# Optimization experiments

Hardware: AMD Instinct MI355X
Metric: run time of the kernel (lower is better)

The kernel has to match this reference:

```python
import jax, jax.numpy as jnp
import numpy as np
import math

B, L, NV, PRED = 8, 512, 32, 96
D, PL, STRIDE = 128, 16, 8
E, TOPN, H = 8, 2, 512
P = (L - PL) // STRIDE + 2  # 64 patches (includes replication pad of STRIDE)
BAL_COEF, Z_COEF = 0.01, 0.001


def sinusoid_pe(n, d):
    pos = np.arange(n, dtype=np.float32)[:, None]
    div = np.exp(np.arange(0, d, 2, dtype=np.float32) * -(math.log(10000.0) / d))
    pe = np.zeros((n, d), dtype=np.float32)
    pe[:, 0::2] = np.sin(pos * div)
    pe[:, 1::2] = np.cos(pos * div)
    return jnp.asarray(pe)


def setup_inputs() -> dict:
    key = jax.random.key(0)
    ks = jax.random.split(key, 10)
    return {
        "x_enc": jax.random.normal(ks[0], (B, L, NV), jnp.float32),
        "x_mark_enc": jax.random.normal(ks[1], (B, L, 4), jnp.float32),
        "x_dec": jnp.zeros((B, 144, NV), jnp.float32),
        "x_mark_dec": jnp.zeros((B, 144, 4), jnp.float32),
        "W_patch": jax.random.normal(ks[2], (PL, D), jnp.float32) * 0.05,
        "Wg": jax.random.normal(ks[3], (D, E), jnp.float32) * 0.05,
        "W1": jax.random.normal(ks[4], (E, D, H), jnp.float32) * 0.05,
        "b1": jnp.zeros((E, H), jnp.float32),
        "W2": jax.random.normal(ks[5], (E, H, D), jnp.float32) * 0.05,
        "b2": jnp.zeros((E, D), jnp.float32),
        "W_head": jax.random.normal(ks[6], (D * P, PRED), jnp.float32) * 0.02,
        "b_head": jnp.zeros((PRED,), jnp.float32),
    }


def _forward(x_enc, W_patch, Wg, W1, b1, W2, b2, W_head, b_head):
    # instance norm over time (detached stats, like the torch code)
    means = jax.lax.stop_gradient(jnp.mean(x_enc, axis=1, keepdims=True))
    xc = x_enc - means
    stdev = jax.lax.stop_gradient(
        jnp.sqrt(jnp.mean((x_enc - means) ** 2, axis=1, keepdims=True) + 1e-5))
    xc = xc / stdev
    # [B, NV, L] -> replication pad right by STRIDE -> unfold into patches
    x = jnp.transpose(xc, (0, 2, 1))
    xp = jnp.pad(x, ((0, 0), (0, 0), (0, STRIDE)), mode="edge")
    idx = jnp.arange(P)[:, None] * STRIDE + jnp.arange(PL)[None, :]  # [P, PL]
    patches = xp[:, :, idx]  # [B, NV, P, PL]
    tok = patches.reshape(B * NV, P, PL)
    h = jnp.einsum("tpl,ld->tpd", tok, W_patch) + sinusoid_pe(P, D)[None]
    # ---- MoE over flattened tokens ----
    N = B * NV * P
    xf = h.reshape(N, D)
    logits = xf @ Wg                              # [N, E]
    probs = jax.nn.softmax(logits, axis=-1)
    gates, tops = jax.lax.top_k(probs, TOPN)      # [N, TOPN]
    # dense per-expert FFN (exact GELU, as nn.GELU default)
    eh = jax.nn.gelu(jnp.einsum("nd,edh->neh", xf, W1) + b1, approximate=False)
    eo = jnp.einsum("neh,ehd->ned", eh, W2) + b2  # [N, E, D]
    onehot = jax.nn.one_hot(tops, E, dtype=xf.dtype)          # [N, TOPN, E]
    cw = jnp.einsum("nk,nke->ne", gates, onehot)              # combine weights
    y = jnp.einsum("ne,ned->nd", cw, eo)
    # aux losses: load-balance + router z-loss
    mask = onehot.sum(axis=1)                                  # [N, E]
    balance = E * jnp.sum(jnp.mean(probs, axis=0) * jnp.mean(mask, axis=0)) / TOPN
    zloss = jnp.mean(jax.nn.logsumexp(logits, axis=-1) ** 2)
    aux = BAL_COEF * balance + Z_COEF * zloss
    # ---- head ----
    enc = y.reshape(B, NV, P, D).transpose(0, 1, 3, 2)         # [B, NV, D, P]
    flat = enc.reshape(B, NV, D * P)
    dec = flat @ W_head + b_head                               # [B, NV, PRED]
    dec = jnp.transpose(dec, (0, 2, 1))                        # [B, PRED, NV]
    dec = dec * stdev[:, 0, :][:, None, :] + means[:, 0, :][:, None, :]
    return dec, aux


def reference(x_enc, x_mark_enc, x_dec, x_mark_dec, W_patch, Wg, W1, b1, W2, b2,
              W_head, b_head):
    return _forward(x_enc, W_patch, Wg, W1, b1, W2, b2, W_head, b_head)
```

## Files before the change

### kernel.cpp

```cpp
#include <hip/hip_runtime.h>
#include <math.h>


typedef __attribute__((ext_vector_type(8))) short bf16x8;
typedef __attribute__((ext_vector_type(4))) float f32x4;

__device__ __forceinline__ float bf2f(unsigned short u){
  unsigned x = ((unsigned)u) << 16; float f; __builtin_memcpy(&f, &x, 4); return f;
}
__device__ __forceinline__ unsigned short f2bf(float f){
  unsigned x; __builtin_memcpy(&x, &f, 4);
  return (unsigned short)((x + 0x7FFFu + ((x >> 16) & 1u)) >> 16);
}
__device__ __forceinline__ float ldin(const void* p, int i, int f32){
  return f32 ? ((const float*)p)[i] : bf2f(((const unsigned short*)p)[i]);
}
__device__ __forceinline__ void stout(void* p, int i, float v, int f32){
  if (f32) ((float*)p)[i] = v; else ((unsigned short*)p)[i] = f2bf(v);
}
__device__ __forceinline__ f32x4 mfma16(bf16x8 a, bf16x8 b, f32x4 c){
  return __builtin_amdgcn_mfma_f32_16x16x32_bf16(a, b, c, 0, 0, 0);
}
#define BAR_RAW() asm volatile("s_waitcnt lgkmcnt(0)\n\ts_barrier" ::: "memory")
__device__ __forceinline__ float gelu_fast(float v){
  float u = v*v;
  float inner = v * fmaf(0.044715f, u, 1.0f);
  float e = __expf(-1.5957691216f * inner);
  return v / (1.0f + e);
}

#define OFF_CNT    0
#define OFF_SUMS   64
#define OFF_MEANS  256
#define OFF_STDS   1280
#define OFF_ECNT   2304
#define OFF_PE     3328
#define OFF_W1T    134400
#define OFF_W2T    1182976
#define OFF_WHT    2231552
#define OFF_CW     3804416
#define OFF_XFBF   4328704
#define OFF_FLATB  8523008
#define OFF_EO     12717312
#define OFF_TOKSLOT 79826176
#define OFF_DECP   79957248

__global__ __launch_bounds__(256) void k_detect(const unsigned short* __restrict__ xe,
                                                int* cnt){
  __shared__ int sc;
  int t = threadIdx.x;
  if (t == 0) sc = 0;
  __syncthreads();
  int c = 0;
  int base = blockIdx.x * 2048;
  for (int k = 0; k < 8; ++k){
    unsigned short u = xe[base + k*256 + t];
    int ex = (u >> 7) & 0xFF;
    if (ex == 0xFF || (ex == 0 && (u & 0x7F))) c++;
  }
  atomicAdd(&sc, c);
  __syncthreads();
  if (t == 0 && sc) atomicAdd(cnt, sc);
}

__global__ __launch_bounds__(256) void k_prep_tr(const void* __restrict__ W1,
                                                 const void* __restrict__ W2,
                                                 const void* __restrict__ Wh,
                                                 const int* cnt, float* pe,
                                                 unsigned short* W1T, unsigned short* W2T,
                                                 unsigned short* WhT){
  int t = threadIdx.x;
  if (blockIdx.x == 0){
    for (int i = t; i < 8192; i += 256){
      int p = i >> 7, d = i & 127;
      float freq = __expf(-(float)(d & ~1) * 0.07195578415606394f);
      float ang = (float)p * freq;
      pe[i] = (d & 1) ? __cosf(ang) : __sinf(ang);
    }
    return;
  }
  int f32 = (cnt[0] >= 4);
  __shared__ float tile[32*33];
  int tb = blockIdx.x - 1;
  int r = t >> 3, cg = (t & 7) * 4;
  const void* src; unsigned short* dst;
  int in0, instride, out0, outstride;
  if (tb < 512){
    int e = tb >> 6, ti = tb & 63, d0 = (ti & 3) * 32, h0 = (ti >> 2) * 32;
    src = W1; dst = W1T;
    in0 = e*65536 + d0*512 + h0; instride = 512;
    out0 = e*65536 + h0*128 + d0; outstride = 128;
  } else if (tb < 1024){
    int tc = tb - 512;
    int e = tc >> 6, ti = tc & 63, d0 = (ti & 3) * 32, h0 = (ti >> 2) * 32;
    src = W2; dst = W2T;
    in0 = e*65536 + h0*128 + d0; instride = 128;
    out0 = e*65536 + d0*512 + h0; outstride = 512;
  } else {
    int tc = tb - 1024;
    int kt = tc / 3, nt = tc - kt*3;
    int k0 = kt*32, n0 = nt*32;
    src = Wh; dst = WhT;
    in0 = k0*96 + n0; instride = 96;
    out0 = n0*8192 + k0; outstride = 8192;
  }
  #pragma unroll
  for (int j = 0; j < 4; ++j)
    tile[r*33 + cg + j] = ldin(src, in0 + r*instride + cg + j, f32);
  __syncthreads();
  ushort4 o;
  o.x = f2bf(tile[(cg+0)*33 + r]);
  o.y = f2bf(tile[(cg+1)*33 + r]);
  o.z = f2bf(tile[(cg+2)*33 + r]);
  o.w = f2bf(tile[(cg+3)*33 + r]);
  *(ushort4*)(dst + out0 + r*outstride + cg) = o;
}

__global__ __launch_bounds__(256) void k_embed(const void* __restrict__ xe,
                                               const void* __restrict__ Wp,
                                               const void* __restrict__ Wg,
                                               const int* cnt,
                                               const float* __restrict__ peg,
                                               float* means, float* stds,
                                               unsigned short* xfbf, float* cwg,
                                               float* sums,
                                               int* ecnt, int* elist, int* tokslot){
  __shared__ float xn[512];
  __shared__ float WpL[2048];
  __shared__ float WgL[1024];
  __shared__ float Xf[8192];
  __shared__ float lp[1024];
  __shared__ float taux[576];
  __shared__ float reds[256], redss[256];
  __shared__ float msh[2];
  __shared__ int lcnt[8], lbase[8];

  int bv = blockIdx.x;
  int b = bv >> 5, v = bv & 31;
  int t = threadIdx.x;
  int f32 = (cnt[0] >= 4);

  if (t < 8) lcnt[t] = 0;

  float x0 = ldin(xe, (b*512 + t)*32 + v, f32);
  float x1 = ldin(xe, (b*512 + t + 256)*32 + v, f32);
  xn[t] = x0; xn[t+256] = x1;
  reds[t] = x0 + x1; redss[t] = x0*x0 + x1*x1;
  #pragma unroll
  for (int it = 0; it < 8; ++it)
    WpL[it*256 + t] = ldin(Wp, it*256 + t, f32);
  #pragma unroll
  for (int j = 0; j < 4; ++j)
    WgL[j*256 + t] = ldin(Wg, j*256 + t, f32);
  __syncthreads();
  for (int s = 128; s > 0; s >>= 1){
    if (t < s){ reds[t] += reds[t+s]; redss[t] += redss[t+s]; }
    __syncthreads();
  }
  if (t == 0){
    float m = reds[0] / 512.f;
    float sd = sqrtf(redss[0] / 512.f - m*m + 1e-5f);
    msh[0] = m; msh[1] = 1.f / sd;
    means[bv] = m; stds[bv] = sd;
  }
  __syncthreads();
  float mean = msh[0], rstd = msh[1];
  xn[t] = (xn[t] - mean) * rstd;
  xn[t+256] = (xn[t+256] - mean) * rstd;
  __syncthreads();
  {
    int p = t >> 2, q = t & 3;
    float tv[16];
    #pragma unroll
    for (int l = 0; l < 16; ++l){
      int xi = p*8 + l; if (xi > 511) xi = 511;
      tv[l] = xn[xi];
    }
    for (int dd = 0; dd < 32; ++dd){
      int d = q*32 + dd;
      float acc = peg[p*128 + d];
      #pragma unroll
      for (int l = 0; l < 16; ++l) acc += tv[l] * WpL[l*128 + d];
      Xf[p*128 + d] = acc;
    }
  }
  __syncthreads();
  if (t < 128){
    int p = t >> 1, half = t & 1;
    float s[8] = {0,0,0,0,0,0,0,0};
    for (int d = half*64; d < half*64 + 64; ++d){
      float xv = Xf[p*128 + d];
      #pragma unroll
      for (int e = 0; e < 8; ++e) s[e] += xv * WgL[d*8 + e];
    }
    #pragma unroll
    for (int e = 0; e < 8; ++e) lp[(p*2 + half)*8 + e] = s[e];
  }
  __syncthreads();
  int bi = 0, si = 0, lo0 = 0, lo1 = 0;
  if (t < 64){
    int p = t;
    float lg[8];
    #pragma unroll
    for (int e = 0; e < 8; ++e) lg[e] = lp[(p*2)*8 + e] + lp[(p*2+1)*8 + e];
    float m = lg[0];
    #pragma unroll
    for (int e = 1; e < 8; ++e) m = fmaxf(m, lg[e]);
    float pr[8]; float se = 0.f;
    #pragma unroll
    for (int e = 0; e < 8; ++e){ pr[e] = __expf(lg[e] - m); se += pr[e]; }
    float inv = 1.f / se;
    float lse = m + logf(se);
    #pragma unroll
    for (int e = 0; e < 8; ++e) pr[e] *= inv;
    float best = -1.f;
    #pragma unroll
    for (int e = 0; e < 8; ++e) if (pr[e] > best){ best = pr[e]; bi = e; }
    float sec = -1.f;
    #pragma unroll
    for (int e = 0; e < 8; ++e) if (e != bi && pr[e] > sec){ sec = pr[e]; si = e; }
    #pragma unroll
    for (int e = 0; e < 8; ++e){
      float w = (e == bi) ? best : ((e == si) ? sec : 0.f);
      cwg[(bv*64 + p)*8 + e] = w;
      taux[p*9 + e] = pr[e];
    }
    taux[p*9 + 8] = lse * lse;
    lp[p] = (float)bi; lp[64 + p] = (float)si;
    lo0 = atomicAdd(&lcnt[bi], 1);
    lo1 = atomicAdd(&lcnt[si], 1);
  }
  __syncthreads();
  if (t < 8) lbase[t] = atomicAdd(ecnt + t*32, lcnt[t]);
  __syncthreads();
  if (t < 64){
    int n = bv*64 + t;
    int p0 = lbase[bi] + lo0, p1 = lbase[si] + lo1;
    elist[bi*16384 + p0] = n;
    elist[si*16384 + p1] = n;
    tokslot[n*2]     = (bi << 14) + p0;
    tokslot[n*2 + 1] = (si << 14) + p1;
  }
  if (t < 17){
    float s = 0.f;
    if (t < 8){ for (int p = 0; p < 64; ++p) s += taux[p*9 + t]; }
    else if (t < 16){
      int e = t - 8;
      for (int p = 0; p < 64; ++p)
        s += ((int)lp[p] == e || (int)lp[64+p] == e) ? 1.f : 0.f;
    }
    else { for (int p = 0; p < 64; ++p) s += taux[p*9 + 8]; }
    atomicAdd(sums + t, s);
  }
  #pragma unroll
  for (int pass = 0; pass < 4; ++pass){
    int idx = pass*256 + t;
    int base = idx*8;
    bf16x8 o;
    #pragma unroll
    for (int j = 0; j < 8; ++j) o[j] = (short)f2bf(Xf[base + j]);
    *(bf16x8*)(xfbf + bv*8192 + base) = o;
  }
}

__global__ __launch_bounds__(256, 3) void k_moe(const unsigned short* __restrict__ xfbf,
                                                const unsigned short* __restrict__ W1T,
                                                const unsigned short* __restrict__ W2T,
                                                const void* __restrict__ b1g,
                                                const int* cnt,
                                                const float* __restrict__ cwg,
                                                const int* __restrict__ ecnt,
                                                const int* __restrict__ elist,
                                                float* __restrict__ Eo){
  __shared__ __align__(16) char lds[49664];
  short* Xs  = (short*)(lds);
  short* Bu1 = (short*)(lds + 8704);
  short* Bu2 = (short*)(lds + 26112);
  short* Ag  = (short*)(lds + 44544);
  float* cws = (float*)(lds + 49152);
  int*   lsn = (int*)(lds + 49280);

  int t = threadIdx.x;
  int e = 8, ti = 0;
  {
    int acc = 0, bk = blockIdx.x;
    #pragma unroll
    for (int ee = 0; ee < 8; ++ee){
      int tl = (ecnt[ee*32] + 31) >> 5;
      if (e == 8 && bk < acc + tl){ e = ee; ti = bk - acc; }
      acc += tl;
    }
  }
  if (e == 8) return;
  int cntE = ecnt[e*32];
  int tbase = ti*32;

  int f32 = (cnt[0] >= 4);
  int wave = t >> 6, lane = t & 63;
  int quad = lane >> 4, li = lane & 15;
  int c1 = wave * 16;
  int c2 = wave * 32;

  const unsigned short* W1e = W1T + e*65536;
  const unsigned short* W2e = W2T + e*65536;

  bf16x8 pf1[4], pf2[4];
  #pragma unroll
  for (int pass = 0; pass < 4; ++pass){
    int idx = pass*64 + lane;
    int row = idx >> 4, kg = idx & 15;
    pf1[pass] = *(const bf16x8*)(W1e + (c1 + row)*128 + kg*8);
  }
  #pragma unroll
  for (int pass = 0; pass < 4; ++pass){
    int idx = pass*64 + lane;
    int row = idx >> 3, kg = idx & 7;
    pf2[pass] = *(const bf16x8*)(W2e + (c2 + row)*512 + kg*8);
  }

  if (t < 32){
    int ok = (tbase + t) < cntE;
    int n = ok ? elist[e*16384 + tbase + t] : 0;
    lsn[t] = n;
    cws[t] = ok ? cwg[n*8 + e] : 0.f;
  }
  __syncthreads();
  #pragma unroll
  for (int pass = 0; pass < 2; ++pass){
    int idx = pass*256 + t;
    int row = idx >> 4, kg = idx & 15;
    int n = lsn[row];
    *(bf16x8*)(Xs + row*136 + kg*8) =
      *(const bf16x8*)(xfbf + n*128 + kg*8);
  }
  float cwv[2][4];
  #pragma unroll
  for (int rt = 0; rt < 2; ++rt)
    #pragma unroll
    for (int r = 0; r < 4; ++r)
      cwv[rt][r] = cws[rt*16 + quad*4 + r];
  __syncthreads();

  f32x4 Yacc[2][2];
  #pragma unroll
  for (int a = 0; a < 2; ++a)
    #pragma unroll
    for (int bb = 0; bb < 2; ++bb){ f32x4 z = {0.f,0.f,0.f,0.f}; Yacc[a][bb] = z; }

  for (int hc = 0; hc < 8; ++hc){
    #pragma unroll
    for (int pass = 0; pass < 4; ++pass){
      int idx = pass*64 + lane;
      int row = idx >> 4, kg = idx & 15;
      *(bf16x8*)(Bu1 + (c1 + row)*136 + kg*8) = pf1[pass];
    }
    #pragma unroll
    for (int pass = 0; pass < 4; ++pass){
      int idx = pass*64 + lane;
      int row = idx >> 3, kg = idx & 7;
      *(bf16x8*)(Bu2 + (c2 + row)*72 + kg*8) = pf2[pass];
    }
    float bias = ldin(b1g, e*512 + hc*64 + c1 + li, f32);
    if (hc < 7){
      #pragma unroll
      for (int pass = 0; pass < 4; ++pass){
        int idx = pass*64 + lane;
        int row = idx >> 4, kg = idx & 15;
        pf1[pass] = *(const bf16x8*)(W1e + ((hc+1)*64 + c1 + row)*128 + kg*8);
      }
      #pragma unroll
      for (int pass = 0; pass < 4; ++pass){
        int idx = pass*64 + lane;
        int row = idx >> 3, kg = idx & 7;
        pf2[pass] = *(const bf16x8*)(W2e + (c2 + row)*512 + (hc+1)*64 + kg*8);
      }
    }
    f32x4 acc1[2];
    { f32x4 z = {0.f,0.f,0.f,0.f}; acc1[0] = z; acc1[1] = z; }
    #pragma unroll
    for (int ks = 0; ks < 4; ++ks){
      int kk = ks*32 + quad*8;
      bf16x8 a0 = *(const bf16x8*)(Xs + li*136 + kk);
      bf16x8 a1 = *(const bf16x8*)(Xs + (16 + li)*136 + kk);
      bf16x8 b0 = *(const bf16x8*)(Bu1 + (c1 + li)*136 + kk);
      acc1[0] = mfma16(a0, b0, acc1[0]);
      acc1[1] = mfma16(a1, b0, acc1[1]);
    }
    BAR_RAW();
    #pragma unroll
    for (int rt = 0; rt < 2; ++rt){
      #pragma unroll
      for (int r = 0; r < 4; ++r){
        int row = rt*16 + quad*4 + r;
        float g = gelu_fast(acc1[rt][r] + bias);
        Ag[row*72 + c1 + li] = (short)f2bf(g * cwv[rt][r]);
      }
    }
    BAR_RAW();
    #pragma unroll
    for (int ks = 0; ks < 2; ++ks){
      int kk = ks*32 + quad*8;
      bf16x8 a0 = *(const bf16x8*)(Ag + li*72 + kk);
      bf16x8 a1 = *(const bf16x8*)(Ag + (16 + li)*72 + kk);
      #pragma unroll
      for (int ct = 0; ct < 2; ++ct){
        bf16x8 bb = *(const bf16x8*)(Bu2 + (c2 + ct*16 + li)*72 + kk);
        Yacc[0][ct] = mfma16(a0, bb, Yacc[0][ct]);
        Yacc[1][ct] = mfma16(a1, bb, Yacc[1][ct]);
      }
    }
  }
  #pragma unroll
  for (int ct = 0; ct < 2; ++ct){
    int col = c2 + ct*16 + li;
    #pragma unroll
    for (int rt = 0; rt < 2; ++rt)
      #pragma unroll
      for (int r = 0; r < 4; ++r){
        int row = rt*16 + quad*4 + r;
        if (tbase + row < cntE)
          Eo[(size_t)((e << 14) + tbase + row)*128 + col] = Yacc[rt][ct][r];
      }
  }
}

__global__ __launch_bounds__(256) void k_flat(const float* __restrict__ Eo,
                                              const int* __restrict__ tokslot,
                                              const float* __restrict__ cwg,
                                              const void* __restrict__ b2g,
                                              const int* cnt,
                                              unsigned short* __restrict__ flatb){
  __shared__ float Yl[64*130];
  __shared__ float b2f[1024];
  __shared__ float cwl[512];
  __shared__ int tsl[128];
  int bv = blockIdx.x;
  int t = threadIdx.x;
  int f32 = (cnt[0] >= 4);
  if (t < 64){
    int2 v = *(const int2*)(tokslot + (bv*64 + t)*2);
    tsl[t*2] = v.x; tsl[t*2+1] = v.y;
  }
  #pragma unroll
  for (int j = 0; j < 4; ++j) b2f[j*256 + t] = ldin(b2g, j*256 + t, f32);
  #pragma unroll
  for (int j = 0; j < 2; ++j) cwl[j*256 + t] = cwg[bv*512 + j*256 + t];
  __syncthreads();
  #pragma unroll
  for (int pass = 0; pass < 32; ++pass){
    int idx = pass*256 + t;
    int row = idx >> 7, col = idx & 127;
    Yl[row*130 + col] = Eo[(size_t)tsl[row*2]*128 + col]
                      + Eo[(size_t)tsl[row*2+1]*128 + col];
  }
  __syncthreads();
  int d = t >> 1, ph = (t & 1) * 32;
  float b2c[8];
  #pragma unroll
  for (int e = 0; e < 8; ++e) b2c[e] = b2f[e*128 + d];
  unsigned short ob[32];
  for (int j = 0; j < 32; ++j){
    int p = ph + j;
    float add = 0.f;
    #pragma unroll
    for (int e = 0; e < 8; ++e) add += cwl[p*8 + e] * b2c[e];
    ob[j] = f2bf(Yl[p*130 + d] + add);
  }
  #pragma unroll
  for (int m = 0; m < 4; ++m)
    *(bf16x8*)(flatb + bv*8192 + d*64 + ph + m*8) = *(bf16x8*)(ob + m*8);
}

__global__ __launch_bounds__(256) void k_head(const unsigned short* __restrict__ flatb,
                                              const unsigned short* __restrict__ WhT,
                                              float* __restrict__ dec_part){
  int t = threadIdx.x;
  int mt = blockIdx.x & 15, kc = blockIdx.x >> 4;
  int wave = t >> 6, lane = t & 63, quad = lane >> 4, li = lane & 15;
  int kbase = kc*512 + wave*128;
  f32x4 acc[6];
  #pragma unroll
  for (int nt = 0; nt < 6; ++nt){ f32x4 z = {0.f,0.f,0.f,0.f}; acc[nt] = z; }
  #pragma unroll
  for (int ks = 0; ks < 4; ++ks){
    int k = kbase + ks*32 + quad*8;
    bf16x8 a = *(const bf16x8*)(flatb + (mt*16 + li)*8192 + k);
    #pragma unroll
    for (int nt = 0; nt < 6; ++nt){
      bf16x8 b = *(const bf16x8*)(WhT + (nt*16 + li)*8192 + k);
      acc[nt] = mfma16(a, b, acc[nt]);
    }
  }
  __shared__ float redsh[4][16][96];
  #pragma unroll
  for (int nt = 0; nt < 6; ++nt)
    #pragma unroll
    for (int r = 0; r < 4; ++r)
      redsh[wave][quad*4 + r][nt*16 + li] = acc[nt][r];
  __syncthreads();
  #pragma unroll
  for (int u = 0; u < 6; ++u){
    int o = t*6 + u;
    int row = o / 96, col = o % 96;
    float s = redsh[0][row][col] + redsh[1][row][col] + redsh[2][row][col] + redsh[3][row][col];
    dec_part[kc*24576 + (mt*16 + row)*96 + col] = s;
  }
}

__global__ __launch_bounds__(256) void k_final(const float* __restrict__ dec_part,
                                               const void* __restrict__ bh,
                                               const int* cnt,
                                               const float* __restrict__ means,
                                               const float* __restrict__ stds,
                                               const float* __restrict__ sums,
                                               void* out){
  int o = blockIdx.x*256 + threadIdx.x;
  int f32 = (cnt[0] >= 4);
  int b = o / 3072, rem = o % 3072, j = rem >> 5, v = rem & 31;
  int bv = b*32 + v;
  int idx = bv*96 + j;
  float s = 0.f;
  #pragma unroll
  for (int kc = 0; kc < 16; ++kc) s += dec_part[kc*24576 + idx];
  float val = (s + ldin(bh, j, f32)) * stds[bv] + means[bv];
  stout(out, o, val, f32);
  if (o == 0){
    float bal = 0.f;
    for (int e = 0; e < 8; ++e) bal += (sums[e] / 16384.f) * (sums[8+e] / 16384.f);
    bal = 8.f * bal / 2.f;
    float aux = 0.01f * bal + 0.001f * (sums[16] / 16384.f);
    stout(out, 24576, aux, f32);
  }
}

extern "C" void kernel_launch(void* const* d_in, const int* in_sizes, int n_in,
                              void* d_out, int out_size, void* d_ws, size_t ws_size,
                              hipStream_t stream){
  const void* xe = d_in[0];
  const void* Wp = d_in[4];
  const void* Wg = d_in[5];
  const void* W1 = d_in[6];
  const void* b1 = d_in[7];
  const void* W2 = d_in[8];
  const void* b2 = d_in[9];
  const void* Wh = d_in[10];
  const void* bh = d_in[11];

  char* ws = (char*)d_ws;
  int*   cnt   = (int*)(ws + OFF_CNT);
  float* sums  = (float*)(ws + OFF_SUMS);
  float* means = (float*)(ws + OFF_MEANS);
  float* stds  = (float*)(ws + OFF_STDS);
  int*   ecnt  = (int*)(ws + OFF_ECNT);
  float* pe    = (float*)(ws + OFF_PE);
  unsigned short* W1T   = (unsigned short*)(ws + OFF_W1T);
  unsigned short* W2T   = (unsigned short*)(ws + OFF_W2T);
  unsigned short* WhT   = (unsigned short*)(ws + OFF_WHT);
  float* cw    = (float*)(ws + OFF_CW);
  unsigned short* xfbf  = (unsigned short*)(ws + OFF_XFBF);
  unsigned short* flatb = (unsigned short*)(ws + OFF_FLATB);
  int*   elist = (int*)(ws + OFF_FLATB);
  float* Eo    = (float*)(ws + OFF_EO);
  int*   tokslot = (int*)(ws + OFF_TOKSLOT);
  float* dec_part = (float*)(ws + OFF_DECP);

  hipMemsetAsync(ws, 0, 3328, stream);
  k_detect<<<64, 256, 0, stream>>>((const unsigned short*)xe, cnt);
  k_prep_tr<<<1793, 256, 0, stream>>>(W1, W2, Wh, cnt, pe, W1T, W2T, WhT);
  k_embed<<<256, 256, 0, stream>>>(xe, Wp, Wg, cnt, pe, means, stds,
                                   xfbf, cw, sums, ecnt, elist, tokslot);
  k_moe<<<1032, 256, 0, stream>>>(xfbf, W1T, W2T, b1, cnt, cw, ecnt, elist, Eo);
  k_flat<<<256, 256, 0, stream>>>(Eo, tokslot, cw, b2, cnt, flatb);
  k_head<<<256, 256, 0, stream>>>(flatb, WhT, dec_part);
  k_final<<<96, 256, 0, stream>>>(dec_part, bh, cnt, means, stds, sums, d_out);
}
```

Before: 159.0 us.

## Drop dtype-detect kernel and load MoE weights directly into registers

Removes the k_detect launch and instead picks the fp32/bf16 input path on the host from the input byte size. It also restructures k_moe so W1/W2 fragments and token rows are read straight from global memory into MFMA operand registers, with W1 double-buffered across h-chunks. This drops the LDS staging buffers and one barrier, shrinking shared memory from about 49KB to about 5KB and allowing higher occupancy. In exchange, each wave issues more scattered global loads, and the dtype choice now relies on the input size convention.

Measured after the change: 163.9 us. 1.03x slower.

```diff
diff --git a/kernel.cpp b/kernel.cpp
--- a/kernel.cpp
+++ b/kernel.cpp
@@ -29,7 +29,6 @@
   return v / (1.0f + e);
 }
 
-#define OFF_CNT    0
 #define OFF_SUMS   64
 #define OFF_MEANS  256
 #define OFF_STDS   1280
@@ -45,28 +44,10 @@
 #define OFF_TOKSLOT 79826176
 #define OFF_DECP   79957248
 
-__global__ __launch_bounds__(256) void k_detect(const unsigned short* __restrict__ xe,
-                                                int* cnt){
-  __shared__ int sc;
-  int t = threadIdx.x;
-  if (t == 0) sc = 0;
-  __syncthreads();
-  int c = 0;
-  int base = blockIdx.x * 2048;
-  for (int k = 0; k < 8; ++k){
-    unsigned short u = xe[base + k*256 + t];
-    int ex = (u >> 7) & 0xFF;
-    if (ex == 0xFF || (ex == 0 && (u & 0x7F))) c++;
-  }
-  atomicAdd(&sc, c);
-  __syncthreads();
-  if (t == 0 && sc) atomicAdd(cnt, sc);
-}
-
 __global__ __launch_bounds__(256) void k_prep_tr(const void* __restrict__ W1,
                                                  const void* __restrict__ W2,
                                                  const void* __restrict__ Wh,
-                                                 const int* cnt, float* pe,
+                                                 int f32, float* pe,
                                                  unsigned short* W1T, unsigned short* W2T,
                                                  unsigned short* WhT){
   int t = threadIdx.x;
@@ -79,7 +60,6 @@
     }
     return;
   }
-  int f32 = (cnt[0] >= 4);
   __shared__ float tile[32*33];
   int tb = blockIdx.x - 1;
   int r = t >> 3, cg = (t & 7) * 4;
@@ -119,7 +99,7 @@
 __global__ __launch_bounds__(256) void k_embed(const void* __restrict__ xe,
                                                const void* __restrict__ Wp,
                                                const void* __restrict__ Wg,
-                                               const int* cnt,
+                                               int f32,
                                                const float* __restrict__ peg,
                                                float* means, float* stds,
                                                unsigned short* xfbf, float* cwg,
@@ -138,7 +118,6 @@
   int bv = blockIdx.x;
   int b = bv >> 5, v = bv & 31;
   int t = threadIdx.x;
-  int f32 = (cnt[0] >= 4);
 
   if (t < 8) lcnt[t] = 0;
 
@@ -267,18 +246,14 @@
                                                 const unsigned short* __restrict__ W1T,
                                                 const unsigned short* __restrict__ W2T,
                                                 const void* __restrict__ b1g,
-                                                const int* cnt,
+                                                int f32,
                                                 const float* __restrict__ cwg,
                                                 const int* __restrict__ ecnt,
                                                 const int* __restrict__ elist,
                                                 float* __restrict__ Eo){
-  __shared__ __align__(16) char lds[49664];
-  short* Xs  = (short*)(lds);
-  short* Bu1 = (short*)(lds + 8704);
-  short* Bu2 = (short*)(lds + 26112);
-  short* Ag  = (short*)(lds + 44544);
-  float* cws = (float*)(lds + 49152);
-  int*   lsn = (int*)(lds + 49280);
+  __shared__ __align__(16) short Ag[32*72];
+  __shared__ float cws[32];
+  __shared__ int   lsn[32];
 
   int t = threadIdx.x;
   int e = 8, ti = 0;
@@ -295,7 +270,6 @@
   int cntE = ecnt[e*32];
   int tbase = ti*32;
 
-  int f32 = (cnt[0] >= 4);
   int wave = t >> 6, lane = t & 63;
   int quad = lane >> 4, li = lane & 15;
   int c1 = wave * 16;
@@ -304,19 +278,12 @@
   const unsigned short* W1e = W1T + e*65536;
   const unsigned short* W2e = W2T + e*65536;
 
-  bf16x8 pf1[4], pf2[4];
-  #pragma unroll
-  for (int pass = 0; pass < 4; ++pass){
-    int idx = pass*64 + lane;
-    int row = idx >> 4, kg = idx & 15;
-    pf1[pass] = *(const bf16x8*)(W1e + (c1 + row)*128 + kg*8);
-  }
-  #pragma unroll
-  for (int pass = 0; pass < 4; ++pass){
-    int idx = pass*64 + lane;
-    int row = idx >> 3, kg = idx & 7;
-    pf2[pass] = *(const bf16x8*)(W2e + (c2 + row)*512 + kg*8);
-  }
+  bf16x8 w1f[2][4];
+  float biasv[2];
+  #pragma unroll
+  for (int ks = 0; ks < 4; ++ks)
+    w1f[0][ks] = *(const bf16x8*)(W1e + (c1 + li)*128 + ks*32 + quad*8);
+  biasv[0] = ldin(b1g, e*512 + c1 + li, f32);
 
   if (t < 32){
     int ok = (tbase + t) < cntE;
@@ -324,14 +291,15 @@
     lsn[t] = n;
     cws[t] = ok ? cwg[n*8 + e] : 0.f;
   }
-  __syncthreads();
-  #pragma unroll
-  for (int pass = 0; pass < 2; ++pass){
-    int idx = pass*256 + t;
-    int row = idx >> 4, kg = idx & 15;
-    int n = lsn[row];
-    *(bf16x8*)(Xs + row*136 + kg*8) =
-      *(const bf16x8*)(xfbf + n*128 + kg*8);
+  BAR_RAW();
+
+  int n0 = lsn[li], n1 = lsn[16 + li];
+  bf16x8 a0[4], a1[4];
+  #pragma unroll
+  for (int ks = 0; ks < 4; ++ks){
+    int kk = ks*32 + quad*8;
+    a0[ks] = *(const bf16x8*)(xfbf + n0*128 + kk);
+    a1[ks] = *(const bf16x8*)(xfbf + n1*128 + kk);
   }
   float cwv[2][4];
   #pragma unroll
@@ -339,7 +307,6 @@
     #pragma unroll
     for (int r = 0; r < 4; ++r)
       cwv[rt][r] = cws[rt*16 + quad*4 + r];
-  __syncthreads();
 
   f32x4 Yacc[2][2];
   #pragma unroll
@@ -347,67 +314,48 @@
     #pragma unroll
     for (int bb = 0; bb < 2; ++bb){ f32x4 z = {0.f,0.f,0.f,0.f}; Yacc[a][bb] = z; }
 
+  #pragma unroll
   for (int hc = 0; hc < 8; ++hc){
-    #pragma unroll
-    for (int pass = 0; pass < 4; ++pass){
-      int idx = pass*64 + lane;
-      int row = idx >> 4, kg = idx & 15;
-      *(bf16x8*)(Bu1 + (c1 + row)*136 + kg*8) = pf1[pass];
-    }
-    #pragma unroll
-    for (int pass = 0; pass < 4; ++pass){
-      int idx = pass*64 + lane;
-      int row = idx >> 3, kg = idx & 7;
-      *(bf16x8*)(Bu2 + (c2 + row)*72 + kg*8) = pf2[pass];
-    }
-    float bias = ldin(b1g, e*512 + hc*64 + c1 + li, f32);
+    const int cur = hc & 1, nxt = cur ^ 1;
+    bf16x8 w2f[2][2];
+    #pragma unroll
+    for (int ks = 0; ks < 2; ++ks)
+      #pragma unroll
+      for (int ct = 0; ct < 2; ++ct)
+        w2f[ks][ct] = *(const bf16x8*)(W2e + (c2 + ct*16 + li)*512 + hc*64 + ks*32 + quad*8);
     if (hc < 7){
       #pragma unroll
-      for (int pass = 0; pass < 4; ++pass){
-        int idx = pass*64 + lane;
-        int row = idx >> 4, kg = idx & 15;
-        pf1[pass] = *(const bf16x8*)(W1e + ((hc+1)*64 + c1 + row)*128 + kg*8);
-      }
-      #pragma unroll
-      for (int pass = 0; pass < 4; ++pass){
-        int idx = pass*64 + lane;
-        int row = idx >> 3, kg = idx & 7;
-        pf2[pass] = *(const bf16x8*)(W2e + (c2 + row)*512 + (hc+1)*64 + kg*8);
-      }
-    }
-    f32x4 acc1[2];
-    { f32x4 z = {0.f,0.f,0.f,0.f}; acc1[0] = z; acc1[1] = z; }
+      for (int ks = 0; ks < 4; ++ks)
+        w1f[nxt][ks] = *(const bf16x8*)(W1e + ((hc+1)*64 + c1 + li)*128 + ks*32 + quad*8);
+      biasv[nxt] = ldin(b1g, e*512 + (hc+1)*64 + c1 + li, f32);
+    }
+    f32x4 acc1a = {0.f,0.f,0.f,0.f}, acc1b = {0.f,0.f,0.f,0.f};
     #pragma unroll
     for (int ks = 0; ks < 4; ++ks){
-      int kk = ks*32 + quad*8;
-      bf16x8 a0 = *(const bf16x8*)(Xs + li*136 + kk);
-      bf16x8 a1 = *(const bf16x8*)(Xs + (16 + li)*136 + kk);
-      bf16x8 b0 = *(const bf16x8*)(Bu1 + (c1 + li)*136 + kk);
-      acc1[0] = mfma16(a0, b0, acc1[0]);
-      acc1[1] = mfma16(a1, b0, acc1[1]);
+      acc1a = mfma16(a0[ks], w1f[cur][ks], acc1a);
+      acc1b = mfma16(a1[ks], w1f[cur][ks], acc1b);
     }
     BAR_RAW();
-    #pragma unroll
-    for (int rt = 0; rt < 2; ++rt){
+    {
+      float bias = biasv[cur];
       #pragma unroll
       for (int r = 0; r < 4; ++r){
-        int row = rt*16 + quad*4 + r;
-        float g = gelu_fast(acc1[rt][r] + bias);
-        Ag[row*72 + c1 + li] = (short)f2bf(g * cwv[rt][r]);
+        float g0 = gelu_fast(acc1a[r] + bias);
+        Ag[(quad*4 + r)*72 + c1 + li] = (short)f2bf(g0 * cwv[0][r]);
+        float g1 = gelu_fast(acc1b[r] + bias);
+        Ag[(16 + quad*4 + r)*72 + c1 + li] = (short)f2bf(g1 * cwv[1][r]);
       }
     }
     BAR_RAW();
     #pragma unroll
     for (int ks = 0; ks < 2; ++ks){
       int kk = ks*32 + quad*8;
-      bf16x8 a0 = *(const bf16x8*)(Ag + li*72 + kk);
-      bf16x8 a1 = *(const bf16x8*)(Ag + (16 + li)*72 + kk);
-      #pragma unroll
-      for (int ct = 0; ct < 2; ++ct){
-        bf16x8 bb = *(const bf16x8*)(Bu2 + (c2 + ct*16 + li)*72 + kk);
-        Yacc[0][ct] = mfma16(a0, bb, Yacc[0][ct]);
-        Yacc[1][ct] = mfma16(a1, bb, Yacc[1][ct]);
-      }
+      bf16x8 g0 = *(const bf16x8*)(Ag + li*72 + kk);
+      bf16x8 g1 = *(const bf16x8*)(Ag + (16 + li)*72 + kk);
+      Yacc[0][0] = mfma16(g0, w2f[ks][0], Yacc[0][0]);
+      Yacc[0][1] = mfma16(g0, w2f[ks][1], Yacc[0][1]);
+      Yacc[1][0] = mfma16(g1, w2f[ks][0], Yacc[1][0]);
+      Yacc[1][1] = mfma16(g1, w2f[ks][1], Yacc[1][1]);
     }
   }
   #pragma unroll
@@ -419,7 +367,7 @@
       for (int r = 0; r < 4; ++r){
         int row = rt*16 + quad*4 + r;
         if (tbase + row < cntE)
-          Eo[(size_t)((e << 14) + tbase + row)*128 + col] = Yacc[rt][ct][r];
+          Eo[(size_t)((e << 14) + tbase + row)*128 + col] = (rt ? ((f32x4*)0, Yacc[1][ct]) : Yacc[0][ct])[r];
       }
   }
 }
@@ -428,7 +376,7 @@
                                               const int* __restrict__ tokslot,
                                               const float* __restrict__ cwg,
                                               const void* __restrict__ b2g,
-                                              const int* cnt,
+                                              int f32,
                                               unsigned short* __restrict__ flatb){
   __shared__ float Yl[64*130];
   __shared__ float b2f[1024];
@@ -436,7 +384,6 @@
   __shared__ int tsl[128];
   int bv = blockIdx.x;
   int t = threadIdx.x;
-  int f32 = (cnt[0] >= 4);
   if (t < 64){
     int2 v = *(const int2*)(tokslot + (bv*64 + t)*2);
     tsl[t*2] = v.x; tsl[t*2+1] = v.y;
@@ -509,13 +456,12 @@
 
 __global__ __launch_bounds__(256) void k_final(const float* __restrict__ dec_part,
                                                const void* __restrict__ bh,
-                                               const int* cnt,
+                                               int f32,
                                                const float* __restrict__ means,
                                                const float* __restrict__ stds,
                                                const float* __restrict__ sums,
                                                void* out){
   int o = blockIdx.x*256 + threadIdx.x;
-  int f32 = (cnt[0] >= 4);
   int b = o / 3072, rem = o % 3072, j = rem >> 5, v = rem & 31;
   int bv = b*32 + v;
   int idx = bv*96 + j;
@@ -546,8 +492,10 @@
   const void* Wh = d_in[10];
   const void* bh = d_in[11];
 
+  int f32 = 1;
+  if (in_sizes && n_in > 0 && in_sizes[0] == 262144) f32 = 0;
+
   char* ws = (char*)d_ws;
-  int*   cnt   = (int*)(ws + OFF_CNT);
   float* sums  = (float*)(ws + OFF_SUMS);
   float* means = (float*)(ws + OFF_MEANS);
   float* stds  = (float*)(ws + OFF_STDS);
@@ -565,12 +513,11 @@
   float* dec_part = (float*)(ws + OFF_DECP);
 
   hipMemsetAsync(ws, 0, 3328, stream);
-  k_detect<<<64, 256, 0, stream>>>((const unsigned short*)xe, cnt);
-  k_prep_tr<<<1793, 256, 0, stream>>>(W1, W2, Wh, cnt, pe, W1T, W2T, WhT);
-  k_embed<<<256, 256, 0, stream>>>(xe, Wp, Wg, cnt, pe, means, stds,
+  k_prep_tr<<<1793, 256, 0, stream>>>(W1, W2, Wh, f32, pe, W1T, W2T, WhT);
+  k_embed<<<256, 256, 0, stream>>>(xe, Wp, Wg, f32, pe, means, stds,
                                    xfbf, cw, sums, ecnt, elist, tokslot);
-  k_moe<<<1032, 256, 0, stream>>>(xfbf, W1T, W2T, b1, cnt, cw, ecnt, elist, Eo);
-  k_flat<<<256, 256, 0, stream>>>(Eo, tokslot, cw, b2, cnt, flatb);
+  k_moe<<<1032, 256, 0, stream>>>(xfbf, W1T, W2T, b1, f32, cw, ecnt, elist, Eo);
+  k_flat<<<256, 256, 0, stream>>>(Eo, tokslot, cw, b2, f32, flatb);
   k_head<<<256, 256, 0, stream>>>(flatb, WhT, dec_part);
-  k_final<<<96, 256, 0, stream>>>(dec_part, bh, cnt, means, stds, sums, d_out);
-}
+  k_final<<<96, 256, 0, stream>>>(dec_part, bh, f32, means, stds, sums, d_out);
+}
```
